# Kernel tuning notes

Measured on AMD Instinct MI355X. Metric: run time of the kernel, lower is better.

The kernel has to match this reference:

```python
import jax, jax.numpy as jnp
import numpy as np

LN_EPS = 1e-5

def _layer_norm(x, g, b):
    m = x.mean(-1, keepdims=True)
    v = ((x - m) ** 2).mean(-1, keepdims=True)
    return (x - m) * jax.lax.rsqrt(v + LN_EPS) * g + b

def _gru_cell(x, h, Wih, Whh, bih, bhh):
    # torch.nn.GRUCell convention; gates ordered (r, z, n)
    gi = x @ Wih.T + bih          # [B, 3H]
    gh = h @ Whh.T + bhh          # [B, 3H]
    i_r, i_z, i_n = jnp.split(gi, 3, axis=-1)
    h_r, h_z, h_n = jnp.split(gh, 3, axis=-1)
    r = jax.nn.sigmoid(i_r + h_r)
    z = jax.nn.sigmoid(i_z + h_z)
    n = jnp.tanh(i_n + r * h_n)
    return (1.0 - z) * n + z * h

def setup_inputs() -> dict:
    key = jax.random.key(0)
    ks = jax.random.split(key, 8)
    B, S, H, L, V = 32, 64, 256, 2, 32000
    return {
        "sent": jax.random.randint(ks[0], (B, S), 0, V, dtype=jnp.int32),
        "length": jax.random.randint(ks[1], (B,), 0, S, dtype=jnp.int32),
        "wordvec": jax.random.normal(ks[2], (V, H), dtype=jnp.float32) * 0.02,
        "W_ih": jax.random.normal(ks[3], (L, 3 * H, H), dtype=jnp.float32) * 0.05,
        "W_hh": jax.random.normal(ks[4], (L, 3 * H, H), dtype=jnp.float32) * 0.05,
        "b_ih": jnp.zeros((L, 3 * H), jnp.float32),
        "b_hh": jnp.zeros((L, 3 * H), jnp.float32),
        "ln_gamma": jnp.ones((L, H), jnp.float32),
        "ln_beta": jnp.zeros((L, H), jnp.float32),
        "linear_w": jax.random.normal(ks[5], (V, H), dtype=jnp.float32) * 0.05,
        "linear_b": jnp.zeros((V,), jnp.float32),
    }

def reference(sent, length, wordvec, W_ih, W_hh, b_ih, b_hh,
              ln_gamma, ln_beta, linear_w, linear_b):
    B, S = sent.shape
    L, _, H = W_hh.shape
    emb = wordvec[sent]                       # [B, S, E]
    xs = (jnp.swapaxes(emb[:, :-1], 0, 1),    # [S-1, B, E]
          sent[:, 1:].T)                      # [S-1, B] targets
    h0 = jnp.zeros((L, B, H), emb.dtype)

    def step(carry, inp):
        h_all, loss = carry
        x, tgt = inp
        hidden = x
        new_hs = []
        for j in range(L):  # small fixed layer count
            hn = _layer_norm(hidden, ln_gamma[j], ln_beta[j])
            new_h = _gru_cell(hn, h_all[j], W_ih[j], W_hh[j], b_ih[j], b_hh[j])
            new_hs.append(new_h)
            hidden = new_h + hn  # residual (E == H)
        logits = hidden @ linear_w.T + linear_b          # [B, V]
        logp = jax.nn.log_softmax(logits, axis=-1)
        ce = -jnp.take_along_axis(logp, tgt[:, None], axis=1)[:, 0]
        mask = (tgt != 0).astype(logits.dtype)
        loss = loss + (ce * mask).sum()
        return (jnp.stack(new_hs), loss), logits

    (_, loss_sum), logits_seq = jax.lax.scan(step, (h0, jnp.zeros((), emb.dtype)), xs)
    loss = loss_sum / length.sum().astype(emb.dtype)
    return loss, jnp.swapaxes(logits_seq, 0, 1)  # [B, S-1, V]
```

## Files before the change

kernel.cpp:

```cpp
#include <hip/hip_runtime.h>
#include <stdint.h>

#define LN_EPS 1e-5f

typedef short bf16x8 __attribute__((ext_vector_type(8)));
typedef short bf16x4 __attribute__((ext_vector_type(4)));
typedef float f32x4 __attribute__((ext_vector_type(4)));

__device__ __forceinline__ float b2f(uint16_t v){ return __uint_as_float(((uint32_t)v) << 16); }
__device__ __forceinline__ uint16_t f2b(float f){
    uint32_t u = __float_as_uint(f);
    u += 0x7fffu + ((u >> 16) & 1u);
    return (uint16_t)(u >> 16);
}
__device__ __forceinline__ float sigm(float x){ return 1.f / (1.f + __expf(-x)); }
__device__ __forceinline__ float wred(float v){
    for (int o = 32; o; o >>= 1) v += __shfl_xor(v, o);
    return v;
}
__device__ __forceinline__ void waitflag(int* f){
    while (__hip_atomic_load(f, __ATOMIC_ACQUIRE, __HIP_MEMORY_SCOPE_AGENT) == 0)
        __builtin_amdgcn_s_sleep(1);
}
__device__ __forceinline__ bf16x8 mk8(bf16x4 lo, bf16x4 hi){
    return (bf16x8){lo[0], lo[1], lo[2], lo[3], hi[0], hi[1], hi[2], hi[3]};
}

__global__ void cvt_kernel(const float* __restrict__ src, uint16_t* __restrict__ dst, int n){
    int i = blockIdx.x * blockDim.x + threadIdx.x;
    int stride = gridDim.x * blockDim.x;
    for (; i < n; i += stride) dst[i] = f2b(src[i]);
}

__global__ void init_kernel(const int* __restrict__ length, float* __restrict__ scal){
    if (threadIdx.x == 0 && blockIdx.x == 0){
        int s = 0;
        for (int i = 0; i < 32; i++) s += length[i];
        scal[0] = 0.f;
        scal[1] = (float)s;
    }
}

__global__ __launch_bounds__(256) void embed_ln_kernel(
    const int* __restrict__ sent, const float* __restrict__ wordvec,
    const float* __restrict__ gamma, const float* __restrict__ beta,
    float* __restrict__ hn_f, uint16_t* __restrict__ hn_h)
{
    const int blk = blockIdx.x;
    const int t = blk >> 5, b = blk & 31;
    const int tid = threadIdx.x;
    __shared__ float red[8];
    const int tok = sent[b * 64 + t];
    const float x = wordvec[(size_t)tok * 256 + tid];
    float v = x;
    for (int o = 32; o; o >>= 1) v += __shfl_down(v, o);
    if ((tid & 63) == 0) red[tid >> 6] = v;
    __syncthreads();
    const float m = (red[0] + red[1] + red[2] + red[3]) * (1.f / 256.f);
    const float d = x - m;
    float v2 = d * d;
    for (int o = 32; o; o >>= 1) v2 += __shfl_down(v2, o);
    if ((tid & 63) == 0) red[4 + (tid >> 6)] = v2;
    __syncthreads();
    const float var = (red[4] + red[5] + red[6] + red[7]) * (1.f / 256.f);
    const float hn = d * rsqrtf(var + LN_EPS) * gamma[tid] + beta[tid];
    const size_t off = (size_t)blk * 256 + tid;
    hn_f[off] = hn;
    hn_h[off] = f2b(hn);
}

template <bool REMAP>
__global__ __launch_bounds__(256) void gemm_bt_kernel(
    const uint16_t* __restrict__ A, const uint16_t* __restrict__ B,
    const float* __restrict__ bias, float* __restrict__ C,
    int M, int N)
{
    __shared__ __align__(16) uint16_t As[128 * 72];
    __shared__ __align__(16) uint16_t Bs[128 * 72];
    const int tid = threadIdx.x;
    const int lane = tid & 63, w = tid >> 6;
    const int wr = w >> 1, wc = w & 1;
    const int m0 = blockIdx.x * 128, n0 = blockIdx.y * 128;
    const int lr = lane & 15;
    const int lk = (lane >> 4) * 4;
    const int srow = tid >> 3;
    const int scol = (tid & 7) * 8;

    f32x4 acc[4][4] = {};

    for (int k0 = 0; k0 < 256; k0 += 64){
        __syncthreads();
        for (int p = 0; p < 4; p++){
            const int row = p * 32 + srow;
            uint4 va = make_uint4(0u, 0u, 0u, 0u);
            const int gm = m0 + row;
            if (gm < M) va = *(const uint4*)(A + (size_t)gm * 256 + k0 + scol);
            *(uint4*)(As + row * 72 + scol) = va;
            const uint4 vb = *(const uint4*)(B + (size_t)(n0 + row) * 256 + k0 + scol);
            *(uint4*)(Bs + row * 72 + scol) = vb;
        }
        __syncthreads();
        for (int kk = 0; kk < 64; kk += 32){
            bf16x8 bfr[4];
            for (int ni = 0; ni < 4; ni++){
                const uint16_t* p = Bs + (wc * 64 + ni * 16 + lr) * 72 + kk + lk;
                bfr[ni] = mk8(*(const bf16x4*)p, *(const bf16x4*)(p + 16));
            }
            for (int mi = 0; mi < 4; mi++){
                const uint16_t* p = As + (wr * 64 + mi * 16 + lr) * 72 + kk + lk;
                bf16x8 afr = mk8(*(const bf16x4*)p, *(const bf16x4*)(p + 16));
                for (int ni = 0; ni < 4; ni++)
                    acc[mi][ni] = __builtin_amdgcn_mfma_f32_16x16x32_bf16(afr, bfr[ni], acc[mi][ni], 0, 0, 0);
            }
        }
    }
    for (int mi = 0; mi < 4; mi++){
        const int gr_base = m0 + wr * 64 + mi * 16 + (lane >> 4) * 4;
        for (int ni = 0; ni < 4; ni++){
            const int gc = n0 + wc * 64 + ni * 16 + lr;
            const float bv = bias[gc];
            for (int r = 0; r < 4; r++){
                const int gm = gr_base + r;
                if (gm < M){
                    const size_t orow = REMAP ? (size_t)((gm & 31) * 63 + (gm >> 5)) : (size_t)gm;
                    C[orow * (size_t)N + gc] = acc[mi][ni][r] + bv;
                }
            }
        }
    }
}

__global__ __launch_bounds__(512) void pipeline_kernel(
    const uint16_t* __restrict__ whh0, const uint16_t* __restrict__ wih1,
    const uint16_t* __restrict__ whh1,
    const float* __restrict__ gi0, const float* __restrict__ hn0f,
    const float* __restrict__ bhh0, const float* __restrict__ bih1,
    const float* __restrict__ bhh1,
    const float* __restrict__ g1, const float* __restrict__ be1,
    uint16_t* __restrict__ hn1buf, float* __restrict__ ga1buf,
    uint16_t* __restrict__ hidh, int* __restrict__ flags)
{
    const int bid = blockIdx.x;
    const int g = bid / 3, role = bid - g * 3;
    const int tid = threadIdx.x;
    const int lane = tid & 63, w = tid >> 6;
    const int lr = lane & 15, lk4 = (lane >> 4) * 4;
    __shared__ __align__(16) char smem[51712];

    if (role == 0){
        float*    h0f = (float*)smem;
        uint16_t* h0b = (uint16_t*)(smem + 16384);
        uint16_t* gb  = (uint16_t*)(smem + 24832);
        float*    red = (float*)(smem + 50944);
        for (int i = tid; i < 4096; i += 512) h0f[i] = 0.f;
        for (int i = tid; i < 4224; i += 512) h0b[i] = 0;
        const int u = tid & 255, bl0 = tid >> 8;
        const float bhr = bhh0[u], bhz = bhh0[256 + u], bhn = bhh0[512 + u];
        const float gam = g1[u], bet = be1[u];
        __syncthreads();
        for (int t = 0; t < 63; t++){
            bf16x8 hfrag[8];
            #pragma unroll
            for (int kc = 0; kc < 8; kc++){
                const uint16_t* hp = h0b + lr * 264 + kc * 32 + lk4;
                hfrag[kc] = mk8(*(const bf16x4*)hp, *(const bf16x4*)(hp + 16));
            }
            for (int i = 0; i < 6; i++){
                const int rt = w * 6 + i;
                f32x4 acc = {0.f, 0.f, 0.f, 0.f};
                const uint16_t* wp = whh0 + (size_t)(rt * 16 + lr) * 256 + lk4;
                #pragma unroll
                for (int kc = 0; kc < 8; kc++){
                    bf16x8 afr = mk8(*(const bf16x4*)(wp + kc * 32), *(const bf16x4*)(wp + kc * 32 + 16));
                    acc = __builtin_amdgcn_mfma_f32_16x16x32_bf16(afr, hfrag[kc], acc, 0, 0, 0);
                }
                const int rbase = rt * 16 + (lane >> 4) * 4;
                #pragma unroll
                for (int j = 0; j < 4; j++) gb[(rbase + j) * 17 + lr] = f2b(acc[j]);
            }
            __syncthreads();
            float hv[8];
            #pragma unroll
            for (int p = 0; p < 8; p++){
                const int b = 2 * p + bl0;
                const size_t rowg = (size_t)t * 32 + g * 16 + b;
                const float gar = gi0[rowg * 768 + u];
                const float gaz = gi0[rowg * 768 + 256 + u];
                const float gan = gi0[rowg * 768 + 512 + u];
                const float gbr = b2f(gb[u * 17 + b]);
                const float gbz = b2f(gb[(256 + u) * 17 + b]);
                const float gbn = b2f(gb[(512 + u) * 17 + b]);
                const float r = sigm(gar + gbr + bhr);
                const float z = sigm(gaz + gbz + bhz);
                const float n = tanhf(gan + r * (gbn + bhn));
                const float h0n = (1.f - z) * n + z * h0f[b * 256 + u];
                h0f[b * 256 + u] = h0n;
                h0b[b * 264 + u] = f2b(h0n);
                const float hidv = h0n + hn0f[rowg * 256 + u];
                hv[p] = hidv;
                const float s1 = wred(hidv), s2 = wred(hidv * hidv);
                if (lane == 0){ red[b * 8 + (w & 3)] = s1; red[b * 8 + 4 + (w & 3)] = s2; }
            }
            __syncthreads();
            #pragma unroll
            for (int p = 0; p < 8; p++){
                const int b = 2 * p + bl0;
                const size_t rowg = (size_t)t * 32 + g * 16 + b;
                const float m  = (red[b * 8] + red[b * 8 + 1] + red[b * 8 + 2] + red[b * 8 + 3]) * (1.f / 256.f);
                const float e2 = (red[b * 8 + 4] + red[b * 8 + 5] + red[b * 8 + 6] + red[b * 8 + 7]) * (1.f / 256.f);
                const float rs = rsqrtf(fmaxf(e2 - m * m, 0.f) + LN_EPS);
                const float hn1 = (hv[p] - m) * rs * gam + bet;
                hn1buf[rowg * 256 + u] = f2b(hn1);
            }
            __syncthreads();
            if (tid == 0){
                __threadfence();
                __hip_atomic_store(&flags[g * 64 + t], 1, __ATOMIC_RELEASE, __HIP_MEMORY_SCOPE_AGENT);
            }
        }
    } else if (role == 1){
        for (int t = 0; t < 63; t++){
            if (tid == 0) waitflag(&flags[g * 64 + t]);
            __syncthreads();
            bf16x8 hfrag[8];
            const uint16_t* hp0 = hn1buf + ((size_t)t * 32 + g * 16 + lr) * 256 + lk4;
            #pragma unroll
            for (int kc = 0; kc < 8; kc++)
                hfrag[kc] = mk8(*(const bf16x4*)(hp0 + kc * 32), *(const bf16x4*)(hp0 + kc * 32 + 16));
            for (int i = 0; i < 6; i++){
                const int rt = w * 6 + i;
                f32x4 acc = {0.f, 0.f, 0.f, 0.f};
                const uint16_t* wp = wih1 + (size_t)(rt * 16 + lr) * 256 + lk4;
                #pragma unroll
                for (int kc = 0; kc < 8; kc++){
                    bf16x8 afr = mk8(*(const bf16x4*)(wp + kc * 32), *(const bf16x4*)(wp + kc * 32 + 16));
                    acc = __builtin_amdgcn_mfma_f32_16x16x32_bf16(afr, hfrag[kc], acc, 0, 0, 0);
                }
                const int rbase = rt * 16 + (lane >> 4) * 4;
                float* gp = ga1buf + ((size_t)(t * 2 + g) * 16 + lr) * 768 + rbase;
                *(float4*)gp = make_float4(acc[0], acc[1], acc[2], acc[3]);
            }
            __syncthreads();
            if (tid == 0){
                __threadfence();
                __hip_atomic_store(&flags[128 + g * 64 + t], 1, __ATOMIC_RELEASE, __HIP_MEMORY_SCOPE_AGENT);
            }
        }
    } else {
        float*    h1f = (float*)smem;
        uint16_t* h1b = (uint16_t*)(smem + 16384);
        uint16_t* gb  = (uint16_t*)(smem + 24832);
        for (int i = tid; i < 4096; i += 512) h1f[i] = 0.f;
        for (int i = tid; i < 4224; i += 512) h1b[i] = 0;
        const int u = tid & 255, bl0 = tid >> 8;
        const float bir = bih1[u], biz = bih1[256 + u], bin = bih1[512 + u];
        const float bhr = bhh1[u], bhz = bhh1[256 + u], bhn = bhh1[512 + u];
        __syncthreads();
        for (int t = 0; t < 63; t++){
            bf16x8 hfrag[8];
            #pragma unroll
            for (int kc = 0; kc < 8; kc++){
                const uint16_t* hp = h1b + lr * 264 + kc * 32 + lk4;
                hfrag[kc] = mk8(*(const bf16x4*)hp, *(const bf16x4*)(hp + 16));
            }
            for (int i = 0; i < 6; i++){
                const int rt = w * 6 + i;
                f32x4 acc = {0.f, 0.f, 0.f, 0.f};
                const uint16_t* wp = whh1 + (size_t)(rt * 16 + lr) * 256 + lk4;
                #pragma unroll
                for (int kc = 0; kc < 8; kc++){
                    bf16x8 afr = mk8(*(const bf16x4*)(wp + kc * 32), *(const bf16x4*)(wp + kc * 32 + 16));
                    acc = __builtin_amdgcn_mfma_f32_16x16x32_bf16(afr, hfrag[kc], acc, 0, 0, 0);
                }
                const int rbase = rt * 16 + (lane >> 4) * 4;
                #pragma unroll
                for (int j = 0; j < 4; j++) gb[(rbase + j) * 17 + lr] = f2b(acc[j]);
            }
            if (tid == 0) waitflag(&flags[128 + g * 64 + t]);
            __syncthreads();
            #pragma unroll
            for (int p = 0; p < 8; p++){
                const int b = 2 * p + bl0;
                const size_t rowg = (size_t)t * 32 + g * 16 + b;
                const size_t gbase = ((size_t)(t * 2 + g) * 16 + b) * 768;
                const float gar = ga1buf[gbase + u] + bir;
                const float gaz = ga1buf[gbase + 256 + u] + biz;
                const float gan = ga1buf[gbase + 512 + u] + bin;
                const float gbr = b2f(gb[u * 17 + b]) + bhr;
                const float gbz = b2f(gb[(256 + u) * 17 + b]) + bhz;
                const float gbn = b2f(gb[(512 + u) * 17 + b]) + bhn;
                const float r = sigm(gar + gbr);
                const float z = sigm(gaz + gbz);
                const float n = tanhf(gan + r * gbn);
                const float h1n = (1.f - z) * n + z * h1f[b * 256 + u];
                h1f[b * 256 + u] = h1n;
                h1b[b * 264 + u] = f2b(h1n);
                const float outv = h1n + b2f(hn1buf[rowg * 256 + u]);
                hidh[rowg * 256 + u] = f2b(outv);
            }
            __syncthreads();
        }
    }
}

__global__ __launch_bounds__(256) void ce_kernel(
    const float* __restrict__ logits, const int* __restrict__ sent,
    float* __restrict__ scal)
{
    const int orow = blockIdx.x;
    const int b = orow / 63, t = orow % 63;
    const float* row = logits + (size_t)orow * 32000;
    const int tid = threadIdx.x;
    const int lane = tid & 63, wid = tid >> 6;
    float m = -INFINITY, s = 0.f;
    const float4* r4 = (const float4*)row;
    for (int i = tid; i < 8000; i += 256){
        const float4 vv = r4[i];
        const float x[4] = {vv.x, vv.y, vv.z, vv.w};
        for (int j = 0; j < 4; j++){
            const float nm = fmaxf(m, x[j]);
            s = s * __expf(m - nm) + __expf(x[j] - nm);
            m = nm;
        }
    }
    for (int o = 32; o; o >>= 1){
        const float mo = __shfl_down(m, o);
        const float so = __shfl_down(s, o);
        const float nm = fmaxf(m, mo);
        s = s * __expf(m - nm) + so * __expf(mo - nm);
        m = nm;
    }
    __shared__ float rm[4], rs_[4];
    if (lane == 0){ rm[wid] = m; rs_[wid] = s; }
    __syncthreads();
    if (tid == 0){
        float M2 = rm[0], S2 = rs_[0];
        for (int i = 1; i < 4; i++){
            const float nm = fmaxf(M2, rm[i]);
            S2 = S2 * __expf(M2 - nm) + rs_[i] * __expf(rm[i] - nm);
            M2 = nm;
        }
        const int tgt = sent[b * 64 + t + 1];
        const float lse = M2 + logf(S2);
        const float ce = lse - row[tgt];
        if (tgt != 0) atomicAdd(scal, ce);
    }
}

__global__ void finalize_kernel(const float* __restrict__ scal, float* __restrict__ out){
    if (threadIdx.x == 0 && blockIdx.x == 0) out[0] = scal[0] / scal[1];
}

extern "C" void kernel_launch(void* const* d_in, const int* in_sizes, int n_in,
                              void* d_out, int out_size, void* d_ws, size_t ws_size,
                              hipStream_t stream)
{
    const int*   sent    = (const int*)  d_in[0];
    const int*   length  = (const int*)  d_in[1];
    const float* wordvec = (const float*)d_in[2];
    const float* W_ih    = (const float*)d_in[3];
    const float* W_hh    = (const float*)d_in[4];
    const float* b_ih    = (const float*)d_in[5];
    const float* b_hh    = (const float*)d_in[6];
    const float* ln_g    = (const float*)d_in[7];
    const float* ln_b    = (const float*)d_in[8];
    const float* lin_w   = (const float*)d_in[9];
    const float* lin_b   = (const float*)d_in[10];
    float* out = (float*)d_out;

    char* ws = (char*)d_ws;
    size_t off = 0;
    auto alloc = [&](size_t bytes) -> char* {
        char* p = ws + off;
        off += (bytes + 255) & ~(size_t)255;
        return p;
    };
    uint16_t* wih_h  = (uint16_t*)alloc((size_t)2 * 768 * 256 * 2);
    uint16_t* whh_h  = (uint16_t*)alloc((size_t)2 * 768 * 256 * 2);
    uint16_t* linw_h = (uint16_t*)alloc((size_t)32000 * 256 * 2);
    float*    hn0f   = (float*)   alloc((size_t)2016 * 256 * 4);
    uint16_t* hn0h   = (uint16_t*)alloc((size_t)2016 * 256 * 2);
    float*    gi0    = (float*)   alloc((size_t)2016 * 768 * 4);
    uint16_t* hidh   = (uint16_t*)alloc((size_t)2016 * 256 * 2);
    float*    scal   = (float*)   alloc(256);
    uint16_t* hn1buf = (uint16_t*)alloc((size_t)63 * 32 * 256 * 2);
    float*    ga1buf = (float*)   alloc((size_t)63 * 2 * 16 * 768 * 4);
    int*      flags  = (int*)     alloc(1024);

    hipLaunchKernelGGL(cvt_kernel, dim3(512), dim3(256), 0, stream, W_ih, wih_h, 2 * 768 * 256);
    hipLaunchKernelGGL(cvt_kernel, dim3(512), dim3(256), 0, stream, W_hh, whh_h, 2 * 768 * 256);
    hipLaunchKernelGGL(cvt_kernel, dim3(2048), dim3(256), 0, stream, lin_w, linw_h, 32000 * 256);
    hipLaunchKernelGGL(init_kernel, dim3(1), dim3(1), 0, stream, length, scal);
    hipMemsetAsync(flags, 0, 1024, stream);
    hipLaunchKernelGGL(embed_ln_kernel, dim3(2016), dim3(256), 0, stream,
                       sent, wordvec, ln_g, ln_b, hn0f, hn0h);
    hipLaunchKernelGGL(gemm_bt_kernel<false>, dim3(16, 6), dim3(256), 0, stream,
                       hn0h, wih_h, b_ih, gi0, 2016, 768);

    {
        const uint16_t* whh0p = whh_h;
        const uint16_t* wih1p = wih_h + 768 * 256;
        const uint16_t* whh1p = whh_h + 768 * 256;
        const float* gi0p = gi0;
        const float* hn0fp = hn0f;
        const float* bhh0p = b_hh;
        const float* bih1p = b_ih + 768;
        const float* bhh1p = b_hh + 768;
        const float* g1p = ln_g + 256;
        const float* be1p = ln_b + 256;
        uint16_t* hn1p = hn1buf;
        float* ga1p = ga1buf;
        uint16_t* hidp = hidh;
        int* flagp = flags;
        void* kargs[] = {
            (void*)&whh0p, (void*)&wih1p, (void*)&whh1p,
            (void*)&gi0p, (void*)&hn0fp,
            (void*)&bhh0p, (void*)&bih1p, (void*)&bhh1p,
            (void*)&g1p, (void*)&be1p,
            (void*)&hn1p, (void*)&ga1p, (void*)&hidp, (void*)&flagp
        };
        hipLaunchCooperativeKernel((const void*)pipeline_kernel, dim3(6), dim3(512),
                                   kargs, 0, stream);
    }

    hipLaunchKernelGGL(gemm_bt_kernel<true>, dim3(16, 250), dim3(256), 0, stream,
                       hidh, linw_h, lin_b, out + 1, 2016, 32000);
    hipLaunchKernelGGL(ce_kernel, dim3(2016), dim3(256), 0, stream, out + 1, sent, scal);
    hipLaunchKernelGGL(finalize_kernel, dim3(1), dim3(1), 0, stream, scal, out);
}
```

Before: 991.2 us.

## Fuse recurrent pipeline and vocab GEMM into one persistent cooperative kernel

Merges the six-block GRU pipeline and the output-projection GEMM into a single cooperative kernel of 256 blocks. The extra blocks wait on per-timestep progress counters and compute 128-row logits tiles as soon as enough hidden states exist, overlapping the large vocab GEMM with the serial recurrence. The recurrent blocks now keep their weight fragments in registers instead of reloading them from global memory each step, and exchange data between roles through staged shared memory with relaxed atomics. The cost is higher register pressure, spin-waiting GEMM blocks competing for CUs, and weaker memory ordering (relaxed atomics plus vmcnt waits instead of release/acquire fences).

After: 995.7 us. About the same (+0.4%).

```diff
diff --git a/kernel.cpp b/kernel.cpp
--- a/kernel.cpp
+++ b/kernel.cpp
@@ -6,6 +6,7 @@
 typedef short bf16x8 __attribute__((ext_vector_type(8)));
 typedef short bf16x4 __attribute__((ext_vector_type(4)));
 typedef float f32x4 __attribute__((ext_vector_type(4)));
+typedef unsigned long long u64;
 
 __device__ __forceinline__ float b2f(uint16_t v){ return __uint_as_float(((uint32_t)v) << 16); }
 __device__ __forceinline__ uint16_t f2b(float f){
@@ -18,12 +19,24 @@
     for (int o = 32; o; o >>= 1) v += __shfl_xor(v, o);
     return v;
 }
-__device__ __forceinline__ void waitflag(int* f){
-    while (__hip_atomic_load(f, __ATOMIC_ACQUIRE, __HIP_MEMORY_SCOPE_AGENT) == 0)
-        __builtin_amdgcn_s_sleep(1);
-}
 __device__ __forceinline__ bf16x8 mk8(bf16x4 lo, bf16x4 hi){
     return (bf16x8){lo[0], lo[1], lo[2], lo[3], hi[0], hi[1], hi[2], hi[3]};
+}
+__device__ __forceinline__ u64 ld_u64(const u64* p){
+    return __hip_atomic_load(p, __ATOMIC_RELAXED, __HIP_MEMORY_SCOPE_AGENT);
+}
+__device__ __forceinline__ void st_u64(u64* p, u64 v){
+    __hip_atomic_store(p, v, __ATOMIC_RELAXED, __HIP_MEMORY_SCOPE_AGENT);
+}
+__device__ __forceinline__ float ld_f32(const float* p){
+    return __hip_atomic_load(p, __ATOMIC_RELAXED, __HIP_MEMORY_SCOPE_AGENT);
+}
+__device__ __forceinline__ void wait_ge(int* f, int v){
+    while (__hip_atomic_load(f, __ATOMIC_RELAXED, __HIP_MEMORY_SCOPE_AGENT) < v)
+        __builtin_amdgcn_s_sleep(2);
+}
+__device__ __forceinline__ u64 pk2(float a, float b){
+    union { float f[2]; u64 u; } x; x.f[0] = a; x.f[1] = b; return x.u;
 }
 
 __global__ void cvt_kernel(const float* __restrict__ src, uint16_t* __restrict__ dst, int n){
@@ -69,7 +82,6 @@
     hn_h[off] = f2b(hn);
 }
 
-template <bool REMAP>
 __global__ __launch_bounds__(256) void gemm_bt_kernel(
     const uint16_t* __restrict__ A, const uint16_t* __restrict__ B,
     const float* __restrict__ bias, float* __restrict__ C,
@@ -121,16 +133,13 @@
             const float bv = bias[gc];
             for (int r = 0; r < 4; r++){
                 const int gm = gr_base + r;
-                if (gm < M){
-                    const size_t orow = REMAP ? (size_t)((gm & 31) * 63 + (gm >> 5)) : (size_t)gm;
-                    C[orow * (size_t)N + gc] = acc[mi][ni][r] + bv;
-                }
-            }
-        }
-    }
-}
-
-__global__ __launch_bounds__(512) void pipeline_kernel(
+                if (gm < M) C[(size_t)gm * N + gc] = acc[mi][ni][r] + bv;
+            }
+        }
+    }
+}
+
+__global__ __launch_bounds__(512, 2) void mega_kernel(
     const uint16_t* __restrict__ whh0, const uint16_t* __restrict__ wih1,
     const uint16_t* __restrict__ whh1,
     const float* __restrict__ gi0, const float* __restrict__ hn0f,
@@ -138,165 +147,277 @@
     const float* __restrict__ bhh1,
     const float* __restrict__ g1, const float* __restrict__ be1,
     uint16_t* __restrict__ hn1buf, float* __restrict__ ga1buf,
-    uint16_t* __restrict__ hidh, int* __restrict__ flags)
+    uint16_t* __restrict__ hidh, int* __restrict__ flags,
+    const uint16_t* __restrict__ linw, const float* __restrict__ linb,
+    float* __restrict__ logits)
 {
     const int bid = blockIdx.x;
-    const int g = bid / 3, role = bid - g * 3;
     const int tid = threadIdx.x;
     const int lane = tid & 63, w = tid >> 6;
     const int lr = lane & 15, lk4 = (lane >> 4) * 4;
-    __shared__ __align__(16) char smem[51712];
-
-    if (role == 0){
-        float*    h0f = (float*)smem;
-        uint16_t* h0b = (uint16_t*)(smem + 16384);
-        uint16_t* gb  = (uint16_t*)(smem + 24832);
-        float*    red = (float*)(smem + 50944);
-        for (int i = tid; i < 4096; i += 512) h0f[i] = 0.f;
-        for (int i = tid; i < 4224; i += 512) h0b[i] = 0;
+    __shared__ __align__(16) char smem[59648];
+
+    if (bid < 6){
+        const int g = bid / 3, role = bid - g * 3;
         const int u = tid & 255, bl0 = tid >> 8;
-        const float bhr = bhh0[u], bhz = bhh0[256 + u], bhn = bhh0[512 + u];
-        const float gam = g1[u], bet = be1[u];
-        __syncthreads();
-        for (int t = 0; t < 63; t++){
-            bf16x8 hfrag[8];
+
+        if (role == 0){
+            float*    h0f = (float*)smem;
+            uint16_t* h0b = (uint16_t*)(smem + 16384);
+            uint16_t* gb  = (uint16_t*)(smem + 24832);
+            float*    red = (float*)(smem + 50944);
+            uint16_t* hns = (uint16_t*)(smem + 51456);
+            bf16x8 wf[6][8];
             #pragma unroll
-            for (int kc = 0; kc < 8; kc++){
-                const uint16_t* hp = h0b + lr * 264 + kc * 32 + lk4;
-                hfrag[kc] = mk8(*(const bf16x4*)hp, *(const bf16x4*)(hp + 16));
-            }
             for (int i = 0; i < 6; i++){
-                const int rt = w * 6 + i;
-                f32x4 acc = {0.f, 0.f, 0.f, 0.f};
-                const uint16_t* wp = whh0 + (size_t)(rt * 16 + lr) * 256 + lk4;
+                const uint16_t* wp = whh0 + (size_t)((w * 6 + i) * 16 + lr) * 256 + lk4;
+                #pragma unroll
+                for (int kc = 0; kc < 8; kc++)
+                    wf[i][kc] = mk8(*(const bf16x4*)(wp + kc * 32), *(const bf16x4*)(wp + kc * 32 + 16));
+            }
+            for (int i = tid; i < 4096; i += 512) h0f[i] = 0.f;
+            for (int i = tid; i < 4224; i += 512) h0b[i] = 0;
+            const float bhr = bhh0[u], bhz = bhh0[256 + u], bhn = bhh0[512 + u];
+            const float gam = g1[u], bet = be1[u];
+            __syncthreads();
+            for (int t = 0; t < 63; t++){
+                bf16x8 hfrag[8];
                 #pragma unroll
                 for (int kc = 0; kc < 8; kc++){
-                    bf16x8 afr = mk8(*(const bf16x4*)(wp + kc * 32), *(const bf16x4*)(wp + kc * 32 + 16));
-                    acc = __builtin_amdgcn_mfma_f32_16x16x32_bf16(afr, hfrag[kc], acc, 0, 0, 0);
-                }
-                const int rbase = rt * 16 + (lane >> 4) * 4;
-                #pragma unroll
-                for (int j = 0; j < 4; j++) gb[(rbase + j) * 17 + lr] = f2b(acc[j]);
-            }
+                    const uint16_t* hp = h0b + lr * 264 + kc * 32 + lk4;
+                    hfrag[kc] = mk8(*(const bf16x4*)hp, *(const bf16x4*)(hp + 16));
+                }
+                #pragma unroll
+                for (int i = 0; i < 6; i++){
+                    f32x4 acc = {0.f, 0.f, 0.f, 0.f};
+                    #pragma unroll
+                    for (int kc = 0; kc < 8; kc++)
+                        acc = __builtin_amdgcn_mfma_f32_16x16x32_bf16(wf[i][kc], hfrag[kc], acc, 0, 0, 0);
+                    const int rbase = (w * 6 + i) * 16 + (lane >> 4) * 4;
+                    #pragma unroll
+                    for (int j = 0; j < 4; j++) gb[(rbase + j) * 17 + lr] = f2b(acc[j]);
+                }
+                __syncthreads();
+                #pragma unroll
+                for (int p = 0; p < 8; p++){
+                    const int b = 2 * p + bl0;
+                    const size_t rowg = (size_t)t * 32 + g * 16 + b;
+                    const float gar = gi0[rowg * 768 + u];
+                    const float gaz = gi0[rowg * 768 + 256 + u];
+                    const float gan = gi0[rowg * 768 + 512 + u];
+                    const float gbr = b2f(gb[u * 17 + b]);
+                    const float gbz = b2f(gb[(256 + u) * 17 + b]);
+                    const float gbn = b2f(gb[(512 + u) * 17 + b]);
+                    const float r = sigm(gar + gbr + bhr);
+                    const float z = sigm(gaz + gbz + bhz);
+                    const float n = tanhf(gan + r * (gbn + bhn));
+                    const float h0n = (1.f - z) * n + z * h0f[b * 256 + u];
+                    h0f[b * 256 + u] = h0n;
+                    h0b[b * 264 + u] = f2b(h0n);
+                    const float hidv = h0n + hn0f[rowg * 256 + u];
+                    const float s1 = wred(hidv), s2 = wred(hidv * hidv);
+                    if (lane == 0){ red[b * 8 + (w & 3)] = s1; red[b * 8 + 4 + (w & 3)] = s2; }
+                }
+                __syncthreads();
+                #pragma unroll
+                for (int p = 0; p < 8; p++){
+                    const int b = 2 * p + bl0;
+                    const size_t rowg = (size_t)t * 32 + g * 16 + b;
+                    const float m  = (red[b * 8] + red[b * 8 + 1] + red[b * 8 + 2] + red[b * 8 + 3]) * (1.f / 256.f);
+                    const float e2 = (red[b * 8 + 4] + red[b * 8 + 5] + red[b * 8 + 6] + red[b * 8 + 7]) * (1.f / 256.f);
+                    const float rs = rsqrtf(fmaxf(e2 - m * m, 0.f) + LN_EPS);
+                    const float hidv = h0f[b * 256 + u] + hn0f[rowg * 256 + u];
+                    hns[b * 256 + u] = f2b((hidv - m) * rs * gam + bet);
+                }
+                __syncthreads();
+                u64* dst = (u64*)(hn1buf + ((size_t)t * 32 + g * 16) * 256);
+                const u64* srcl = (const u64*)hns;
+                #pragma unroll
+                for (int q = 0; q < 2; q++) st_u64(dst + tid + q * 512, srcl[tid + q * 512]);
+                asm volatile("s_waitcnt vmcnt(0)" ::: "memory");
+                __syncthreads();
+                if (tid == 0)
+                    __hip_atomic_store(&flags[g * 64 + t], 1, __ATOMIC_RELAXED, __HIP_MEMORY_SCOPE_AGENT);
+            }
+        } else if (role == 1){
+            uint16_t* hns = (uint16_t*)smem;
+            bf16x8 wf[6][8];
+            #pragma unroll
+            for (int i = 0; i < 6; i++){
+                const uint16_t* wp = wih1 + (size_t)((w * 6 + i) * 16 + lr) * 256 + lk4;
+                #pragma unroll
+                for (int kc = 0; kc < 8; kc++)
+                    wf[i][kc] = mk8(*(const bf16x4*)(wp + kc * 32), *(const bf16x4*)(wp + kc * 32 + 16));
+            }
+            for (int t = 0; t < 63; t++){
+                if (tid == 0) wait_ge(&flags[g * 64 + t], 1);
+                __syncthreads();
+                const u64* src = (const u64*)(hn1buf + ((size_t)t * 32 + g * 16) * 256);
+                #pragma unroll
+                for (int q = 0; q < 2; q++){
+                    const int j = tid + q * 512;
+                    const u64 v = ld_u64(src + j);
+                    *(u64*)(hns + (j >> 6) * 264 + (j & 63) * 4) = v;
+                }
+                __syncthreads();
+                bf16x8 hfrag[8];
+                #pragma unroll
+                for (int kc = 0; kc < 8; kc++){
+                    const uint16_t* hp = hns + lr * 264 + kc * 32 + lk4;
+                    hfrag[kc] = mk8(*(const bf16x4*)hp, *(const bf16x4*)(hp + 16));
+                }
+                #pragma unroll
+                for (int i = 0; i < 6; i++){
+                    f32x4 acc = {0.f, 0.f, 0.f, 0.f};
+                    #pragma unroll
+                    for (int kc = 0; kc < 8; kc++)
+                        acc = __builtin_amdgcn_mfma_f32_16x16x32_bf16(wf[i][kc], hfrag[kc], acc, 0, 0, 0);
+                    const int rbase = (w * 6 + i) * 16 + (lane >> 4) * 4;
+                    u64* gp = (u64*)(ga1buf + ((size_t)(t * 2 + g) * 16 + lr) * 768 + rbase);
+                    st_u64(gp,     pk2(acc[0], acc[1]));
+                    st_u64(gp + 1, pk2(acc[2], acc[3]));
+                }
+                asm volatile("s_waitcnt vmcnt(0)" ::: "memory");
+                __syncthreads();
+                if (tid == 0)
+                    __hip_atomic_store(&flags[128 + g * 64 + t], 1, __ATOMIC_RELAXED, __HIP_MEMORY_SCOPE_AGENT);
+            }
+        } else {
+            float*    h1f = (float*)smem;
+            uint16_t* h1b = (uint16_t*)(smem + 16384);
+            uint16_t* gb  = (uint16_t*)(smem + 24832);
+            uint16_t* hnc = (uint16_t*)(smem + 50944);
+            bf16x8 wf[6][8];
+            #pragma unroll
+            for (int i = 0; i < 6; i++){
+                const uint16_t* wp = whh1 + (size_t)((w * 6 + i) * 16 + lr) * 256 + lk4;
+                #pragma unroll
+                for (int kc = 0; kc < 8; kc++)
+                    wf[i][kc] = mk8(*(const bf16x4*)(wp + kc * 32), *(const bf16x4*)(wp + kc * 32 + 16));
+            }
+            for (int i = tid; i < 4096; i += 512) h1f[i] = 0.f;
+            for (int i = tid; i < 4224; i += 512) h1b[i] = 0;
+            const float bir = bih1[u], biz = bih1[256 + u], bin = bih1[512 + u];
+            const float bhr = bhh1[u], bhz = bhh1[256 + u], bhn = bhh1[512 + u];
             __syncthreads();
-            float hv[8];
-            #pragma unroll
-            for (int p = 0; p < 8; p++){
-                const int b = 2 * p + bl0;
-                const size_t rowg = (size_t)t * 32 + g * 16 + b;
-                const float gar = gi0[rowg * 768 + u];
-                const float gaz = gi0[rowg * 768 + 256 + u];
-                const float gan = gi0[rowg * 768 + 512 + u];
-                const float gbr = b2f(gb[u * 17 + b]);
-                const float gbz = b2f(gb[(256 + u) * 17 + b]);
-                const float gbn = b2f(gb[(512 + u) * 17 + b]);
-                const float r = sigm(gar + gbr + bhr);
-                const float z = sigm(gaz + gbz + bhz);
-                const float n = tanhf(gan + r * (gbn + bhn));
-                const float h0n = (1.f - z) * n + z * h0f[b * 256 + u];
-                h0f[b * 256 + u] = h0n;
-                h0b[b * 264 + u] = f2b(h0n);
-                const float hidv = h0n + hn0f[rowg * 256 + u];
-                hv[p] = hidv;
-                const float s1 = wred(hidv), s2 = wred(hidv * hidv);
-                if (lane == 0){ red[b * 8 + (w & 3)] = s1; red[b * 8 + 4 + (w & 3)] = s2; }
-            }
+            for (int t = 0; t < 63; t++){
+                bf16x8 hfrag[8];
+                #pragma unroll
+                for (int kc = 0; kc < 8; kc++){
+                    const uint16_t* hp = h1b + lr * 264 + kc * 32 + lk4;
+                    hfrag[kc] = mk8(*(const bf16x4*)hp, *(const bf16x4*)(hp + 16));
+                }
+                #pragma unroll
+                for (int i = 0; i < 6; i++){
+                    f32x4 acc = {0.f, 0.f, 0.f, 0.f};
+                    #pragma unroll
+                    for (int kc = 0; kc < 8; kc++)
+                        acc = __builtin_amdgcn_mfma_f32_16x16x32_bf16(wf[i][kc], hfrag[kc], acc, 0, 0, 0);
+                    const int rbase = (w * 6 + i) * 16 + (lane >> 4) * 4;
+                    #pragma unroll
+                    for (int j = 0; j < 4; j++) gb[(rbase + j) * 17 + lr] = f2b(acc[j]);
+                }
+                if (tid == 0) wait_ge(&flags[128 + g * 64 + t], 1);
+                __syncthreads();
+                const u64* src = (const u64*)(hn1buf + ((size_t)t * 32 + g * 16) * 256);
+                #pragma unroll
+                for (int q = 0; q < 2; q++){
+                    const int j = tid + q * 512;
+                    *(u64*)(hnc + (j >> 6) * 256 + (j & 63) * 4) = ld_u64(src + j);
+                }
+                __syncthreads();
+                #pragma unroll
+                for (int p = 0; p < 8; p++){
+                    const int b = 2 * p + bl0;
+                    const size_t gbase = ((size_t)(t * 2 + g) * 16 + b) * 768;
+                    const float gar = ld_f32(ga1buf + gbase + u) + bir;
+                    const float gaz = ld_f32(ga1buf + gbase + 256 + u) + biz;
+                    const float gan = ld_f32(ga1buf + gbase + 512 + u) + bin;
+                    const float gbr = b2f(gb[u * 17 + b]) + bhr;
+                    const float gbz = b2f(gb[(256 + u) * 17 + b]) + bhz;
+                    const float gbn = b2f(gb[(512 + u) * 17 + b]) + bhn;
+                    const float r = sigm(gar + gbr);
+                    const float z = sigm(gaz + gbz);
+                    const float n = tanhf(gan + r * gbn);
+                    const float h1n = (1.f - z) * n + z * h1f[b * 256 + u];
+                    h1f[b * 256 + u] = h1n;
+                    h1b[b * 264 + u] = f2b(h1n);
+                    const float outv = h1n + b2f(hnc[b * 256 + u]);
+                    hnc[b * 256 + u] = f2b(outv);
+                }
+                __syncthreads();
+                u64* dst = (u64*)(hidh + ((size_t)t * 32 + g * 16) * 256);
+                const u64* srcl = (const u64*)hnc;
+                #pragma unroll
+                for (int q = 0; q < 2; q++) st_u64(dst + tid + q * 512, srcl[tid + q * 512]);
+                asm volatile("s_waitcnt vmcnt(0)" ::: "memory");
+                __syncthreads();
+                if (tid == 0)
+                    __hip_atomic_store(&flags[256 + g], t + 1, __ATOMIC_RELAXED, __HIP_MEMORY_SCOPE_AGENT);
+            }
+        }
+    } else {
+        uint16_t* As = (uint16_t*)smem;
+        uint16_t* Bs = (uint16_t*)(smem + 18432);
+        const int gb6 = bid - 6;
+        const int ct = gb6 >> 1, par = gb6 & 1;
+        const int n0 = ct * 256;
+        const int wr = w >> 2, wc = w & 3;
+        for (int mt = par; mt < 16; mt += 2){
+            const int need = (mt + 1) * 4 > 63 ? 63 : (mt + 1) * 4;
+            if (tid == 0){ wait_ge(&flags[256], need); wait_ge(&flags[257], need); }
             __syncthreads();
-            #pragma unroll
-            for (int p = 0; p < 8; p++){
-                const int b = 2 * p + bl0;
-                const size_t rowg = (size_t)t * 32 + g * 16 + b;
-                const float m  = (red[b * 8] + red[b * 8 + 1] + red[b * 8 + 2] + red[b * 8 + 3]) * (1.f / 256.f);
-                const float e2 = (red[b * 8 + 4] + red[b * 8 + 5] + red[b * 8 + 6] + red[b * 8 + 7]) * (1.f / 256.f);
-                const float rs = rsqrtf(fmaxf(e2 - m * m, 0.f) + LN_EPS);
-                const float hn1 = (hv[p] - m) * rs * gam + bet;
-                hn1buf[rowg * 256 + u] = f2b(hn1);
-            }
-            __syncthreads();
-            if (tid == 0){
-                __threadfence();
-                __hip_atomic_store(&flags[g * 64 + t], 1, __ATOMIC_RELEASE, __HIP_MEMORY_SCOPE_AGENT);
-            }
-        }
-    } else if (role == 1){
-        for (int t = 0; t < 63; t++){
-            if (tid == 0) waitflag(&flags[g * 64 + t]);
-            __syncthreads();
-            bf16x8 hfrag[8];
-            const uint16_t* hp0 = hn1buf + ((size_t)t * 32 + g * 16 + lr) * 256 + lk4;
-            #pragma unroll
-            for (int kc = 0; kc < 8; kc++)
-                hfrag[kc] = mk8(*(const bf16x4*)(hp0 + kc * 32), *(const bf16x4*)(hp0 + kc * 32 + 16));
-            for (int i = 0; i < 6; i++){
-                const int rt = w * 6 + i;
-                f32x4 acc = {0.f, 0.f, 0.f, 0.f};
-                const uint16_t* wp = wih1 + (size_t)(rt * 16 + lr) * 256 + lk4;
-                #pragma unroll
-                for (int kc = 0; kc < 8; kc++){
-                    bf16x8 afr = mk8(*(const bf16x4*)(wp + kc * 32), *(const bf16x4*)(wp + kc * 32 + 16));
-                    acc = __builtin_amdgcn_mfma_f32_16x16x32_bf16(afr, hfrag[kc], acc, 0, 0, 0);
-                }
-                const int rbase = rt * 16 + (lane >> 4) * 4;
-                float* gp = ga1buf + ((size_t)(t * 2 + g) * 16 + lr) * 768 + rbase;
-                *(float4*)gp = make_float4(acc[0], acc[1], acc[2], acc[3]);
-            }
-            __syncthreads();
-            if (tid == 0){
-                __threadfence();
-                __hip_atomic_store(&flags[128 + g * 64 + t], 1, __ATOMIC_RELEASE, __HIP_MEMORY_SCOPE_AGENT);
-            }
-        }
-    } else {
-        float*    h1f = (float*)smem;
-        uint16_t* h1b = (uint16_t*)(smem + 16384);
-        uint16_t* gb  = (uint16_t*)(smem + 24832);
-        for (int i = tid; i < 4096; i += 512) h1f[i] = 0.f;
-        for (int i = tid; i < 4224; i += 512) h1b[i] = 0;
-        const int u = tid & 255, bl0 = tid >> 8;
-        const float bir = bih1[u], biz = bih1[256 + u], bin = bih1[512 + u];
-        const float bhr = bhh1[u], bhz = bhh1[256 + u], bhn = bhh1[512 + u];
-        __syncthreads();
-        for (int t = 0; t < 63; t++){
-            bf16x8 hfrag[8];
-            #pragma unroll
-            for (int kc = 0; kc < 8; kc++){
-                const uint16_t* hp = h1b + lr * 264 + kc * 32 + lk4;
-                hfrag[kc] = mk8(*(const bf16x4*)hp, *(const bf16x4*)(hp + 16));
-            }
-            for (int i = 0; i < 6; i++){
-                const int rt = w * 6 + i;
-                f32x4 acc = {0.f, 0.f, 0.f, 0.f};
-                const uint16_t* wp = whh1 + (size_t)(rt * 16 + lr) * 256 + lk4;
-                #pragma unroll
-                for (int kc = 0; kc < 8; kc++){
-                    bf16x8 afr = mk8(*(const bf16x4*)(wp + kc * 32), *(const bf16x4*)(wp + kc * 32 + 16));
-                    acc = __builtin_amdgcn_mfma_f32_16x16x32_bf16(afr, hfrag[kc], acc, 0, 0, 0);
-                }
-                const int rbase = rt * 16 + (lane >> 4) * 4;
-                #pragma unroll
-                for (int j = 0; j < 4; j++) gb[(rbase + j) * 17 + lr] = f2b(acc[j]);
-            }
-            if (tid == 0) waitflag(&flags[128 + g * 64 + t]);
-            __syncthreads();
-            #pragma unroll
-            for (int p = 0; p < 8; p++){
-                const int b = 2 * p + bl0;
-                const size_t rowg = (size_t)t * 32 + g * 16 + b;
-                const size_t gbase = ((size_t)(t * 2 + g) * 16 + b) * 768;
-                const float gar = ga1buf[gbase + u] + bir;
-                const float gaz = ga1buf[gbase + 256 + u] + biz;
-                const float gan = ga1buf[gbase + 512 + u] + bin;
-                const float gbr = b2f(gb[u * 17 + b]) + bhr;
-                const float gbz = b2f(gb[(256 + u) * 17 + b]) + bhz;
-                const float gbn = b2f(gb[(512 + u) * 17 + b]) + bhn;
-                const float r = sigm(gar + gbr);
-                const float z = sigm(gaz + gbz);
-                const float n = tanhf(gan + r * gbn);
-                const float h1n = (1.f - z) * n + z * h1f[b * 256 + u];
-                h1f[b * 256 + u] = h1n;
-                h1b[b * 264 + u] = f2b(h1n);
-                const float outv = h1n + b2f(hn1buf[rowg * 256 + u]);
-                hidh[rowg * 256 + u] = f2b(outv);
+            const int m0 = mt * 128;
+            f32x4 acc[4][4] = {};
+            for (int k0 = 0; k0 < 256; k0 += 64){
+                __syncthreads();
+                #pragma unroll
+                for (int q = 0; q < 4; q++){
+                    const int j = tid + q * 512;
+                    const int row = j >> 4, uc = (j & 15) * 4;
+                    const int gm = m0 + row;
+                    u64 v = 0;
+                    if (gm < 2016) v = ld_u64((const u64*)(hidh + (size_t)gm * 256 + k0) + (j & 15));
+                    *(u64*)(As + row * 72 + uc) = v;
+                }
+                #pragma unroll
+                for (int q = 0; q < 4; q++){
+                    const int j = tid + q * 512;
+                    const int row = j >> 3, sc = (j & 7) * 8;
+                    *(uint4*)(Bs + row * 72 + sc) =
+                        *(const uint4*)(linw + (size_t)(n0 + row) * 256 + k0 + sc);
+                }
+                __syncthreads();
+                for (int kk = 0; kk < 64; kk += 32){
+                    bf16x8 bfr[4];
+                    #pragma unroll
+                    for (int ni = 0; ni < 4; ni++){
+                        const uint16_t* p = Bs + (wc * 64 + ni * 16 + lr) * 72 + kk + lk4;
+                        bfr[ni] = mk8(*(const bf16x4*)p, *(const bf16x4*)(p + 16));
+                    }
+                    #pragma unroll
+                    for (int mi = 0; mi < 4; mi++){
+                        const uint16_t* p = As + (wr * 64 + mi * 16 + lr) * 72 + kk + lk4;
+                        bf16x8 afr = mk8(*(const bf16x4*)p, *(const bf16x4*)(p + 16));
+                        #pragma unroll
+                        for (int ni = 0; ni < 4; ni++)
+                            acc[mi][ni] = __builtin_amdgcn_mfma_f32_16x16x32_bf16(afr, bfr[ni], acc[mi][ni], 0, 0, 0);
+                    }
+                }
+            }
+            for (int mi = 0; mi < 4; mi++){
+                const int gr_base = m0 + wr * 64 + mi * 16 + (lane >> 4) * 4;
+                for (int ni = 0; ni < 4; ni++){
+                    const int gc = n0 + wc * 64 + ni * 16 + lr;
+                    const float bv = linb[gc];
+                    for (int r = 0; r < 4; r++){
+                        const int gm = gr_base + r;
+                        if (gm < 2016){
+                            const size_t orow = (size_t)((gm & 31) * 63 + (gm >> 5));
+                            logits[orow * 32000 + gc] = acc[mi][ni][r] + bv;
+                        }
+                    }
+                }
             }
             __syncthreads();
         }
@@ -385,16 +506,16 @@
     float*    scal   = (float*)   alloc(256);
     uint16_t* hn1buf = (uint16_t*)alloc((size_t)63 * 32 * 256 * 2);
     float*    ga1buf = (float*)   alloc((size_t)63 * 2 * 16 * 768 * 4);
-    int*      flags  = (int*)     alloc(1024);
+    int*      flags  = (int*)     alloc(4096);
 
     hipLaunchKernelGGL(cvt_kernel, dim3(512), dim3(256), 0, stream, W_ih, wih_h, 2 * 768 * 256);
     hipLaunchKernelGGL(cvt_kernel, dim3(512), dim3(256), 0, stream, W_hh, whh_h, 2 * 768 * 256);
     hipLaunchKernelGGL(cvt_kernel, dim3(2048), dim3(256), 0, stream, lin_w, linw_h, 32000 * 256);
     hipLaunchKernelGGL(init_kernel, dim3(1), dim3(1), 0, stream, length, scal);
-    hipMemsetAsync(flags, 0, 1024, stream);
+    hipMemsetAsync(flags, 0, 4096, stream);
     hipLaunchKernelGGL(embed_ln_kernel, dim3(2016), dim3(256), 0, stream,
                        sent, wordvec, ln_g, ln_b, hn0f, hn0h);
-    hipLaunchKernelGGL(gemm_bt_kernel<false>, dim3(16, 6), dim3(256), 0, stream,
+    hipLaunchKernelGGL(gemm_bt_kernel, dim3(16, 6), dim3(256), 0, stream,
                        hn0h, wih_h, b_ih, gi0, 2016, 768);
 
     {
@@ -412,19 +533,21 @@
         float* ga1p = ga1buf;
         uint16_t* hidp = hidh;
         int* flagp = flags;
+        const uint16_t* linwp = linw_h;
+        const float* linbp = lin_b;
+        float* logp = out + 1;
         void* kargs[] = {
             (void*)&whh0p, (void*)&wih1p, (void*)&whh1p,
             (void*)&gi0p, (void*)&hn0fp,
             (void*)&bhh0p, (void*)&bih1p, (void*)&bhh1p,
             (void*)&g1p, (void*)&be1p,
-            (void*)&hn1p, (void*)&ga1p, (void*)&hidp, (void*)&flagp
+            (void*)&hn1p, (void*)&ga1p, (void*)&hidp, (void*)&flagp,
+            (void*)&linwp, (void*)&linbp, (void*)&logp
         };
-        hipLaunchCooperativeKernel((const void*)pipeline_kernel, dim3(6), dim3(512),
+        hipLaunchCooperativeKernel((const void*)mega_kernel, dim3(256), dim3(512),
                                    kargs, 0, stream);
     }
 
-    hipLaunchKernelGGL(gemm_bt_kernel<true>, dim3(16, 250), dim3(256), 0, stream,
-                       hidh, linw_h, lin_b, out + 1, 2016, 32000);
     hipLaunchKernelGGL(ce_kernel, dim3(2016), dim3(256), 0, stream, out + 1, sent, scal);
     hipLaunchKernelGGL(finalize_kernel, dim3(1), dim3(1), 0, stream, scal, out);
 }
```
